# Performance work log

Hardware: AMD Instinct MI355X
Metric: run time of the kernel (lower is better)

Reference implementation:

```python
import jax, jax.numpy as jnp
import numpy as np

EMBED = 1024
HEAD = 128
B, T = 4, 4096


def setup_inputs() -> dict:
    key = jax.random.key(0)
    k1, k2, k3, k4 = jax.random.split(key, 4)
    context = jax.random.normal(k1, (B, T, EMBED), dtype=jnp.float32)
    # nn.Linear(embedding_size, head_size, bias=False): y = x @ W^T; store W^T as [C, H]
    s = 1.0 / np.sqrt(EMBED)
    Wk = jax.random.normal(k2, (EMBED, HEAD), dtype=jnp.float32) * s
    Wq = jax.random.normal(k3, (EMBED, HEAD), dtype=jnp.float32) * s
    Wv = jax.random.normal(k4, (EMBED, HEAD), dtype=jnp.float32) * s
    return {"context": context, "Wk": Wk, "Wq": Wq, "Wv": Wv}


def reference(context, Wk, Wq, Wv):
    Bc, Tc, C = context.shape
    k = jnp.einsum("btc,ch->bth", context, Wk)
    q = jnp.einsum("btc,ch->bth", context, Wq)
    v = jnp.einsum("btc,ch->bth", context, Wv)
    # NOTE: original scales by 1/sqrt(C) (embedding size), not 1/sqrt(head_size)
    scale = 1.0 / jnp.sqrt(jnp.float32(C))
    scores = jnp.einsum("bqh,bkh->bqk", q, k) * scale  # [B, T, T]
    causal = jnp.tril(jnp.ones((Tc, Tc), dtype=bool))
    scores = jnp.where(causal, scores, -jnp.inf)
    attn = jax.nn.softmax(scores, axis=-1)
    # dropout_rate = 0.0 (eval-mode): no-op
    out = jnp.einsum("bqk,bkh->bqh", attn, v)
    return out
```

## Files before the change

kernel.cpp:

```cpp
#include <hip/hip_runtime.h>
#include <cstdint>
#include <cstddef>

#define EMBED 1024
#define HEAD  128
#define BATCH 4
#define SEQ   4096
#define KSC   0.04508422f

typedef __attribute__((ext_vector_type(4))) float f32x4;
typedef __attribute__((ext_vector_type(16))) float f32x16;
typedef __attribute__((ext_vector_type(8))) short s16x8;
typedef __attribute__((ext_vector_type(4))) int i32x4;
typedef __attribute__((ext_vector_type(4))) unsigned short u16x4;

__device__ __forceinline__ unsigned short f2bf(float f) {
    union { float f; unsigned u; } v; v.f = f;
    unsigned r = v.u + 0x7fffu + ((v.u >> 16) & 1u);
    return (unsigned short)(r >> 16);
}

__device__ __forceinline__ int cvtpk(float lo, float hi_) {
    int r;
    asm("v_cvt_pk_bf16_f32 %0, %1, %2" : "=v"(r) : "v"(lo), "v"(hi_));
    return r;
}

__device__ __forceinline__ void gload16(const void* g, void* l) {
    __builtin_amdgcn_global_load_lds(
        (const __attribute__((address_space(1))) unsigned int*)g,
        (__attribute__((address_space(3))) unsigned int*)l, 16, 0, 0);
}

__global__ __launch_bounds__(256) void wt_kernel(const float* __restrict__ Wq,
                                                 const float* __restrict__ Wk,
                                                 const float* __restrict__ Wv,
                                                 unsigned short* __restrict__ Wt) {
    __shared__ __align__(16) float Lw[64 * 132];
    const int tid = threadIdx.x;
    const int sel = blockIdx.x >> 4;
    const int kb  = blockIdx.x & 15;
    const int k0  = kb * 64;
    const float* W = (sel == 0) ? Wq : (sel == 1) ? Wk : Wv;
    #pragma unroll
    for (int it = 0; it < 8; ++it) {
        int c = tid + it * 256;
        int kk = c >> 5, hc = c & 31;
        *(f32x4*)&Lw[kk * 132 + hc * 4] =
            *(const f32x4*)(W + (size_t)(k0 + kk) * HEAD + hc * 4);
    }
    __syncthreads();
    #pragma unroll
    for (int it = 0; it < 4; ++it) {
        int c = tid + it * 256;
        int h = c >> 3, sl = c & 7;
        int phys = sl ^ (h & 7);
        int p0 = cvtpk(Lw[(sl * 8 + 0) * 132 + h], Lw[(sl * 8 + 1) * 132 + h]);
        int p1 = cvtpk(Lw[(sl * 8 + 2) * 132 + h], Lw[(sl * 8 + 3) * 132 + h]);
        int p2 = cvtpk(Lw[(sl * 8 + 4) * 132 + h], Lw[(sl * 8 + 5) * 132 + h]);
        int p3 = cvtpk(Lw[(sl * 8 + 6) * 132 + h], Lw[(sl * 8 + 7) * 132 + h]);
        i32x4 pk = {p0, p1, p2, p3};
        *(s16x8*)(Wt + (size_t)sel * 131072 + kb * 8192 + h * 64 + phys * 8) = *(s16x8*)&pk;
    }
}

__global__ __launch_bounds__(512) void proj_kernel(const float* __restrict__ ctx,
                                                   const unsigned short* __restrict__ Wt,
                                                   unsigned short* __restrict__ Qb,
                                                   unsigned short* __restrict__ Kb,
                                                   unsigned short* __restrict__ Vtb) {
    __shared__ __align__(16) short As[64 * 72];
    __shared__ __align__(16) short Bs[3 * 128 * 64];
    const int tid = threadIdx.x;
    const int lane = tid & 63, w = tid >> 6;
    const int wr = w >> 2, wc = w & 3;
    const int lr = lane & 15, lk = lane >> 4;
    const int m0 = blockIdx.x * 64;

    f32x4 zero = {0.f, 0.f, 0.f, 0.f};
    f32x4 acc[2][6];
    #pragma unroll
    for (int i = 0; i < 2; ++i)
        #pragma unroll
        for (int jn = 0; jn < 6; ++jn) acc[i][jn] = zero;

    for (int kb = 0; kb < 16; ++kb) {
        __syncthreads();
        #pragma unroll
        for (int i = 0; i < 6; ++i) {
            int c = w * 6 + i;
            int sel = c >> 4, within = c & 15;
            gload16((const char*)Wt + sel * 262144 + kb * 16384 + within * 1024 + lane * 16,
                    (char*)Bs + c * 1024);
        }
        {
            int row = tid >> 3, cg = tid & 7;
            const float* src = ctx + (size_t)(m0 + row) * EMBED + kb * 64 + cg * 8;
            f32x4 x0 = *(const f32x4*)src;
            f32x4 x1 = *(const f32x4*)(src + 4);
            int p0 = cvtpk(x0[0], x0[1]);
            int p1 = cvtpk(x0[2], x0[3]);
            int p2 = cvtpk(x1[0], x1[1]);
            int p3 = cvtpk(x1[2], x1[3]);
            i32x4 pk = {p0, p1, p2, p3};
            *(s16x8*)&As[row * 72 + cg * 8] = *(s16x8*)&pk;
        }
        __syncthreads();
        #pragma unroll
        for (int k2 = 0; k2 < 2; ++k2) {
            s16x8 af[2], bfr[6];
            #pragma unroll
            for (int mi = 0; mi < 2; ++mi)
                af[mi] = *(const s16x8*)&As[(wr * 32 + mi * 16 + lr) * 72 + k2 * 32 + lk * 8];
            #pragma unroll
            for (int ni = 0; ni < 6; ++ni) {
                int col = wc * 96 + ni * 16 + lr;
                int sel = col >> 7, rB = col & 127;
                int phys = (k2 * 4 + lk) ^ (rB & 7);
                bfr[ni] = *(const s16x8*)(Bs + sel * 8192 + rB * 64 + phys * 8);
            }
            #pragma unroll
            for (int mi = 0; mi < 2; ++mi)
                #pragma unroll
                for (int ni = 0; ni < 6; ++ni)
                    acc[mi][ni] = __builtin_amdgcn_mfma_f32_16x16x32_bf16(af[mi], bfr[ni], acc[mi][ni], 0, 0, 0);
        }
    }

    #pragma unroll
    for (int mi = 0; mi < 2; ++mi) {
        int rowBase = m0 + wr * 32 + mi * 16 + lk * 4;
        #pragma unroll
        for (int ni = 0; ni < 6; ++ni) {
            int col = wc * 96 + ni * 16 + lr;
            int sel = col >> 7, cIn = col & 127;
            if (sel == 2) {
                int b = rowBase >> 12, tl = rowBase & (SEQ - 1);
                u16x4 vv;
                #pragma unroll
                for (int r = 0; r < 4; ++r) vv[r] = f2bf(acc[mi][ni][r]);
                *(u16x4*)(Vtb + ((size_t)(b * HEAD + cIn)) * SEQ + tl) = vv;
            } else {
                unsigned short* outp = sel ? Kb : Qb;
                float sc = sel ? 1.0f : KSC;
                #pragma unroll
                for (int r = 0; r < 4; ++r)
                    outp[(size_t)(rowBase + r) * HEAD + cIn] = f2bf(acc[mi][ni][r] * sc);
            }
        }
    }
}

__global__ __launch_bounds__(256, 2) void attn_kernel(const unsigned short* __restrict__ Q,
                                                      const unsigned short* __restrict__ K,
                                                      const unsigned short* __restrict__ Vt,
                                                      unsigned short* __restrict__ po,
                                                      float* __restrict__ pml) {
    __shared__ __align__(16) char smem[32768];
    const int tid = threadIdx.x;
    const int lane = tid & 63, w = tid >> 6;
    const int l31 = lane & 31, hi = lane >> 5;
    const int hi16 = hi << 4;

    const int b = blockIdx.x / 272;
    int t = blockIdx.x % 272;
    int qt = 0, cum = 0;
    while (cum + ((qt >> 1) + 1) <= t) { cum += (qt >> 1) + 1; ++qt; }
    const int c = t - cum;
    const int nj = min(4, 2 * qt + 2 - 4 * c);
    const int kb0 = c * 256;
    const int slot = b * 272 + cum + c;

    const unsigned short* qp = Q + ((size_t)(b * SEQ + qt * 128 + w * 32 + l31)) * HEAD + hi * 8;
    s16x8 qf[8];
    #pragma unroll
    for (int dt = 0; dt < 8; ++dt) qf[dt] = *(const s16x8*)(qp + dt * 16);

    f32x16 o0, o1, o2, o3;
    #pragma unroll
    for (int r = 0; r < 16; ++r) { o0[r] = 0.f; o1[r] = 0.f; o2[r] = 0.f; o3[r] = 0.f; }
    float m_run = -1e30f, l_run = 0.f;

    const int krow = tid >> 4, kch = tid & 15;
    const int vdr  = tid >> 3, vch = tid & 7;

    s16x8 kst[4], vst[4];
    #pragma unroll
    for (int p = 0; p < 4; ++p) {
        kst[p] = *(const s16x8*)(K + ((size_t)(b * SEQ + kb0 + krow + p * 16)) * HEAD + kch * 8);
        vst[p] = *(const s16x8*)(Vt + ((size_t)(b * HEAD + vdr + p * 32)) * SEQ + kb0 + vch * 8);
    }
    #pragma unroll
    for (int p = 0; p < 4; ++p) {
        int r0 = krow + p * 16;
        *(s16x8*)(smem + r0 * 256 + ((kch * 16) ^ ((r0 & 7) << 4))) = kst[p];
        int d0 = vdr + p * 32;
        *(s16x8*)(smem + 16384 + d0 * 128 + ((vch * 16) ^ ((d0 & 7) << 4))) = vst[p];
    }
    __syncthreads();

    for (int j = 0; j < nj; ++j) {
        const int kb = kb0 + j * 64;
        if (j + 1 < nj) {
            int kbn = kb + 64;
            #pragma unroll
            for (int p = 0; p < 4; ++p) {
                kst[p] = *(const s16x8*)(K + ((size_t)(b * SEQ + kbn + krow + p * 16)) * HEAD + kch * 8);
                vst[p] = *(const s16x8*)(Vt + ((size_t)(b * HEAD + vdr + p * 32)) * SEQ + kbn + vch * 8);
            }
        }

        f32x16 st0, st1;
        #pragma unroll
        for (int r = 0; r < 16; ++r) { st0[r] = 0.f; st1[r] = 0.f; }
        const int sw = (l31 & 7) << 4;
        const char* kbase0 = smem + l31 * 256;
        const char* kbase1 = kbase0 + 32 * 256;
        __builtin_amdgcn_s_setprio(1);
        #pragma unroll
        for (int dt = 0; dt < 8; ++dt) {
            s16x8 ka0 = *(const s16x8*)(kbase0 + ((dt * 32 + hi16) ^ sw));
            s16x8 ka1 = *(const s16x8*)(kbase1 + ((dt * 32 + hi16) ^ sw));
            st0 = __builtin_amdgcn_mfma_f32_32x32x16_bf16(ka0, qf[dt], st0, 0, 0, 0);
            st1 = __builtin_amdgcn_mfma_f32_32x32x16_bf16(ka1, qf[dt], st1, 0, 0, 0);
        }
        __builtin_amdgcn_s_setprio(0);

        if (4 * c + j >= 2 * qt) {
            const int qg = qt * 128 + w * 32 + l31;
            #pragma unroll
            for (int r = 0; r < 16; ++r) {
                int crow = (r & 3) + 8 * (r >> 2) + 4 * hi;
                if (kb + crow > qg)      st0[r] = -3e37f;
                if (kb + 32 + crow > qg) st1[r] = -3e37f;
            }
        }

        float mx = st0[0];
        #pragma unroll
        for (int r = 1; r < 16; ++r) mx = fmaxf(mx, st0[r]);
        #pragma unroll
        for (int r = 0; r < 16; ++r) mx = fmaxf(mx, st1[r]);
        mx = fmaxf(mx, __shfl_xor(mx, 32));
        if (!__all(mx <= m_run + 8.0f)) {
            float mn = fmaxf(m_run, mx);
            float f = exp2f(m_run - mn);
            l_run *= f;
            int fi = __float_as_int(f);
            #pragma unroll
            for (int r = 0; r < 16; ++r) {
                int srcb = 4 * ((r & 3) + 8 * (r >> 2)) + 16 * hi;
                float fr = __int_as_float(__builtin_amdgcn_ds_bpermute(srcb, fi));
                o0[r] *= fr; o1[r] *= fr; o2[r] *= fr; o3[r] *= fr;
            }
            m_run = mn;
        }
        float rs = 0.f;
        #pragma unroll
        for (int r = 0; r < 16; ++r) {
            st0[r] = exp2f(st0[r] - m_run); rs += st0[r];
            st1[r] = exp2f(st1[r] - m_run); rs += st1[r];
        }
        rs += __shfl_xor(rs, 32);
        l_run += rs;

        int a0 = cvtpk(st0[0], st0[1]),   b0 = cvtpk(st0[4], st0[5]);
        int a1 = cvtpk(st0[2], st0[3]),   b1 = cvtpk(st0[6], st0[7]);
        int a2 = cvtpk(st0[8], st0[9]),   b2 = cvtpk(st0[12], st0[13]);
        int a3 = cvtpk(st0[10], st0[11]), b3 = cvtpk(st0[14], st0[15]);
        int a4 = cvtpk(st1[0], st1[1]),   b4 = cvtpk(st1[4], st1[5]);
        int a5 = cvtpk(st1[2], st1[3]),   b5 = cvtpk(st1[6], st1[7]);
        int a6 = cvtpk(st1[8], st1[9]),   b6 = cvtpk(st1[12], st1[13]);
        int a7 = cvtpk(st1[10], st1[11]), b7 = cvtpk(st1[14], st1[15]);
        asm volatile("v_permlane32_swap_b32 %0, %1" : "+v"(a0), "+v"(b0));
        asm volatile("v_permlane32_swap_b32 %0, %1" : "+v"(a1), "+v"(b1));
        asm volatile("v_permlane32_swap_b32 %0, %1" : "+v"(a2), "+v"(b2));
        asm volatile("v_permlane32_swap_b32 %0, %1" : "+v"(a3), "+v"(b3));
        asm volatile("v_permlane32_swap_b32 %0, %1" : "+v"(a4), "+v"(b4));
        asm volatile("v_permlane32_swap_b32 %0, %1" : "+v"(a5), "+v"(b5));
        asm volatile("v_permlane32_swap_b32 %0, %1" : "+v"(a6), "+v"(b6));
        asm volatile("v_permlane32_swap_b32 %0, %1" : "+v"(a7), "+v"(b7));
        i32x4 pw0 = {a0, a1, b0, b1}; s16x8 pa0 = *(s16x8*)&pw0;
        i32x4 pw1 = {a2, a3, b2, b3}; s16x8 pa1 = *(s16x8*)&pw1;
        i32x4 pw2 = {a4, a5, b4, b5}; s16x8 pa2 = *(s16x8*)&pw2;
        i32x4 pw3 = {a6, a7, b6, b7}; s16x8 pa3 = *(s16x8*)&pw3;

        __builtin_amdgcn_s_setprio(1);
        #define PV_NT(oo, nt) { \
            const int vr = (nt) * 32 + l31; \
            const int vsw = (vr & 7) << 4; \
            const char* vb = smem + 16384 + vr * 128; \
            oo = __builtin_amdgcn_mfma_f32_32x32x16_bf16(pa0, *(const s16x8*)(vb + ((0  + hi16) ^ vsw)), oo, 0, 0, 0); \
            oo = __builtin_amdgcn_mfma_f32_32x32x16_bf16(pa1, *(const s16x8*)(vb + ((32 + hi16) ^ vsw)), oo, 0, 0, 0); \
            oo = __builtin_amdgcn_mfma_f32_32x32x16_bf16(pa2, *(const s16x8*)(vb + ((64 + hi16) ^ vsw)), oo, 0, 0, 0); \
            oo = __builtin_amdgcn_mfma_f32_32x32x16_bf16(pa3, *(const s16x8*)(vb + ((96 + hi16) ^ vsw)), oo, 0, 0, 0); }
        PV_NT(o0, 0) PV_NT(o1, 1) PV_NT(o2, 2) PV_NT(o3, 3)
        #undef PV_NT
        __builtin_amdgcn_s_setprio(0);

        if (j + 1 < nj) {
            __syncthreads();
            #pragma unroll
            for (int p = 0; p < 4; ++p) {
                int r0 = krow + p * 16;
                *(s16x8*)(smem + r0 * 256 + ((kch * 16) ^ ((r0 & 7) << 4))) = kst[p];
                int d0 = vdr + p * 32;
                *(s16x8*)(smem + 16384 + d0 * 128 + ((vch * 16) ^ ((d0 & 7) << 4))) = vst[p];
            }
            __syncthreads();
        }
    }

    __syncthreads();
    short* os = (short*)smem;
    #define STORE_NT(oo, nt) { \
        _Pragma("unroll") \
        for (int r = 0; r < 16; ++r) { \
            int qin = w * 32 + (r & 3) + 8 * (r >> 2) + 4 * hi; \
            os[qin * 128 + (nt) * 32 + l31] = (short)f2bf(oo[r]); \
        } }
    STORE_NT(o0, 0) STORE_NT(o1, 1) STORE_NT(o2, 2) STORE_NT(o3, 3)
    #undef STORE_NT
    unsigned short* pob = po + (size_t)slot * 16384 + w * 4096;
    const short* osw = os + w * 4096;
    #pragma unroll
    for (int jj = 0; jj < 8; ++jj) {
        s16x8 v = *(const s16x8*)(osw + jj * 512 + lane * 8);
        *(s16x8*)(pob + jj * 512 + lane * 8) = v;
    }
    if (lane < 32) {
        float* pm = pml + (size_t)slot * 256 + (w * 32 + lane) * 2;
        pm[0] = m_run; pm[1] = l_run;
    }
}

__global__ __launch_bounds__(256) void combine_kernel(const unsigned short* __restrict__ po,
                                                      const float* __restrict__ pml,
                                                      float* __restrict__ out) {
    const int tid = threadIdx.x;
    const int row = blockIdx.x * 8 + (tid >> 5);
    const int l32 = tid & 31;
    const int b = row >> 12, q = row & 4095;
    const int qt = q >> 7, qr = q & 127;
    const int nc = (q >> 8) + 1;
    const int cum = ((qt >> 1) + (qt & 1)) * ((qt >> 1) + 1);
    const size_t bslot = (size_t)b * 272 + cum;

    float M = -1e30f;
    for (int cc = 0; cc < nc; ++cc)
        M = fmaxf(M, pml[(bslot + cc) * 256 + qr * 2]);
    float L = 0.f;
    f32x4 acc = {0.f, 0.f, 0.f, 0.f};
    for (int cc = 0; cc < nc; ++cc) {
        const float* pm = pml + (bslot + cc) * 256 + qr * 2;
        float wgt = exp2f(pm[0] - M);
        L += wgt * pm[1];
        u16x4 x = *(const u16x4*)(po + (bslot + cc) * 16384 + qr * 128 + l32 * 4);
        #pragma unroll
        for (int e = 0; e < 4; ++e) {
            union { unsigned u; float f; } cv; cv.u = ((unsigned)x[e]) << 16;
            acc[e] += wgt * cv.f;
        }
    }
    float inv = 1.f / L;
    f32x4 y = {acc[0] * inv, acc[1] * inv, acc[2] * inv, acc[3] * inv};
    *(f32x4*)(out + (size_t)row * HEAD + l32 * 4) = y;
}

extern "C" void kernel_launch(void* const* d_in, const int* in_sizes, int n_in,
                              void* d_out, int out_size, void* d_ws, size_t ws_size,
                              hipStream_t stream) {
    const float* ctx = (const float*)d_in[0];
    const float* Wk  = (const float*)d_in[1];
    const float* Wq  = (const float*)d_in[2];
    const float* Wv  = (const float*)d_in[3];
    float* out = (float*)d_out;

    unsigned short* Wt  = (unsigned short*)d_ws;
    unsigned short* Qb  = Wt + 3 * 131072;
    unsigned short* Kb  = Qb + 2097152;
    unsigned short* Vtb = Kb + 2097152;
    unsigned short* po  = Vtb + 2097152;
    float* pml = (float*)(po + (size_t)1088 * 16384);

    wt_kernel<<<48, 256, 0, stream>>>(Wq, Wk, Wv, Wt);
    proj_kernel<<<256, 512, 0, stream>>>(ctx, Wt, Qb, Kb, Vtb);
    attn_kernel<<<1088, 256, 0, stream>>>(Qb, Kb, Vtb, po, pml);
    combine_kernel<<<2048, 256, 0, stream>>>(po, pml, out);
}
```

Before: 171.8 us.

## Fuse split-KV combine into attention via atomic ticket, widen KV chunks

Each attention block now covers up to 512 keys instead of 256, cutting the split count per batch from 272 to 144 work items. The separate combine kernel is removed. The last block to finish a query tile, detected with an atomic counter (reset in wt_kernel), merges the partial outputs and writes the final fp32 result. This removes a kernel launch and some partial-result traffic. The cost is fewer blocks to fill the machine, longer critical-path blocks, and a serial merge tail inside one block per query tile.

```diff
diff --git a/kernel.cpp b/kernel.cpp
--- a/kernel.cpp
+++ b/kernel.cpp
@@ -35,9 +35,11 @@
 __global__ __launch_bounds__(256) void wt_kernel(const float* __restrict__ Wq,
                                                  const float* __restrict__ Wk,
                                                  const float* __restrict__ Wv,
-                                                 unsigned short* __restrict__ Wt) {
+                                                 unsigned short* __restrict__ Wt,
+                                                 int* __restrict__ cnt) {
     __shared__ __align__(16) float Lw[64 * 132];
     const int tid = threadIdx.x;
+    if (blockIdx.x == 0 && tid < 128) cnt[tid] = 0;
     const int sel = blockIdx.x >> 4;
     const int kb  = blockIdx.x & 15;
     const int k0  = kb * 64;
@@ -155,21 +157,25 @@
                                                       const unsigned short* __restrict__ K,
                                                       const unsigned short* __restrict__ Vt,
                                                       unsigned short* __restrict__ po,
-                                                      float* __restrict__ pml) {
+                                                      float* __restrict__ pml,
+                                                      int* __restrict__ cnt,
+                                                      float* __restrict__ out) {
     __shared__ __align__(16) char smem[32768];
+    __shared__ int ticket;
     const int tid = threadIdx.x;
     const int lane = tid & 63, w = tid >> 6;
     const int l31 = lane & 31, hi = lane >> 5;
     const int hi16 = hi << 4;
 
-    const int b = blockIdx.x / 272;
-    int t = blockIdx.x % 272;
-    int qt = 0, cum = 0;
-    while (cum + ((qt >> 1) + 1) <= t) { cum += (qt >> 1) + 1; ++qt; }
+    const int b = blockIdx.x / 144;
+    int t = blockIdx.x % 144;
+    int qt = 0, cum = 0, nc = 1;
+    while (cum + nc <= t) { cum += nc; ++qt; nc = (qt >> 2) + 1; }
     const int c = t - cum;
-    const int nj = min(4, 2 * qt + 2 - 4 * c);
-    const int kb0 = c * 256;
-    const int slot = b * 272 + cum + c;
+    const int nj = min(8, 2 * qt + 2 - 8 * c);
+    const int kb0 = c * 512;
+    const int gbase = b * 144 + cum;
+    const int slot = gbase + c;
 
     const unsigned short* qp = Q + ((size_t)(b * SEQ + qt * 128 + w * 32 + l31)) * HEAD + hi * 8;
     s16x8 qf[8];
@@ -226,7 +232,7 @@
         }
         __builtin_amdgcn_s_setprio(0);
 
-        if (4 * c + j >= 2 * qt) {
+        if (8 * c + j >= 2 * qt) {
             const int qg = qt * 128 + w * 32 + l31;
             #pragma unroll
             for (int r = 0; r < 16; ++r) {
@@ -332,39 +338,36 @@
         float* pm = pml + (size_t)slot * 256 + (w * 32 + lane) * 2;
         pm[0] = m_run; pm[1] = l_run;
     }
-}
-
-__global__ __launch_bounds__(256) void combine_kernel(const unsigned short* __restrict__ po,
-                                                      const float* __restrict__ pml,
-                                                      float* __restrict__ out) {
-    const int tid = threadIdx.x;
-    const int row = blockIdx.x * 8 + (tid >> 5);
-    const int l32 = tid & 31;
-    const int b = row >> 12, q = row & 4095;
-    const int qt = q >> 7, qr = q & 127;
-    const int nc = (q >> 8) + 1;
-    const int cum = ((qt >> 1) + (qt & 1)) * ((qt >> 1) + 1);
-    const size_t bslot = (size_t)b * 272 + cum;
-
-    float M = -1e30f;
-    for (int cc = 0; cc < nc; ++cc)
-        M = fmaxf(M, pml[(bslot + cc) * 256 + qr * 2]);
-    float L = 0.f;
-    f32x4 acc = {0.f, 0.f, 0.f, 0.f};
-    for (int cc = 0; cc < nc; ++cc) {
-        const float* pm = pml + (bslot + cc) * 256 + qr * 2;
-        float wgt = exp2f(pm[0] - M);
-        L += wgt * pm[1];
-        u16x4 x = *(const u16x4*)(po + (bslot + cc) * 16384 + qr * 128 + l32 * 4);
-        #pragma unroll
-        for (int e = 0; e < 4; ++e) {
-            union { unsigned u; float f; } cv; cv.u = ((unsigned)x[e]) << 16;
-            acc[e] += wgt * cv.f;
-        }
-    }
-    float inv = 1.f / L;
-    f32x4 y = {acc[0] * inv, acc[1] * inv, acc[2] * inv, acc[3] * inv};
-    *(f32x4*)(out + (size_t)row * HEAD + l32 * 4) = y;
+
+    __threadfence();
+    if (tid == 0) ticket = atomicAdd(&cnt[b * 32 + qt], 1);
+    __syncthreads();
+    if (ticket == nc - 1) {
+        __threadfence();
+        const int colg = (tid & 31) * 4;
+        for (int it = 0; it < 16; ++it) {
+            int row = it * 8 + (tid >> 5);
+            float M = -1e30f;
+            for (int cc = 0; cc < nc; ++cc)
+                M = fmaxf(M, pml[(size_t)(gbase + cc) * 256 + row * 2]);
+            float L = 0.f;
+            f32x4 acc = {0.f, 0.f, 0.f, 0.f};
+            for (int cc = 0; cc < nc; ++cc) {
+                const float* pm = pml + (size_t)(gbase + cc) * 256 + row * 2;
+                float wgt = exp2f(pm[0] - M);
+                L += wgt * pm[1];
+                u16x4 x = *(const u16x4*)(po + (size_t)(gbase + cc) * 16384 + row * 128 + colg);
+                #pragma unroll
+                for (int e = 0; e < 4; ++e) {
+                    union { unsigned u; float f; } cv; cv.u = ((unsigned)x[e]) << 16;
+                    acc[e] += wgt * cv.f;
+                }
+            }
+            float inv = 1.f / L;
+            f32x4 y = {acc[0] * inv, acc[1] * inv, acc[2] * inv, acc[3] * inv};
+            *(f32x4*)(out + (size_t)(b * SEQ + qt * 128 + row) * HEAD + colg) = y;
+        }
+    }
 }
 
 extern "C" void kernel_launch(void* const* d_in, const int* in_sizes, int n_in,
@@ -381,10 +384,10 @@
     unsigned short* Kb  = Qb + 2097152;
     unsigned short* Vtb = Kb + 2097152;
     unsigned short* po  = Vtb + 2097152;
-    float* pml = (float*)(po + (size_t)1088 * 16384);
-
-    wt_kernel<<<48, 256, 0, stream>>>(Wq, Wk, Wv, Wt);
+    float* pml = (float*)(po + (size_t)576 * 16384);
+    int* cnt   = (int*)(pml + (size_t)576 * 256);
+
+    wt_kernel<<<48, 256, 0, stream>>>(Wq, Wk, Wv, Wt, cnt);
     proj_kernel<<<256, 512, 0, stream>>>(ctx, Wt, Qb, Kb, Vtb);
-    attn_kernel<<<1088, 256, 0, stream>>>(Qb, Kb, Vtb, po, pml);
-    combine_kernel<<<2048, 256, 0, stream>>>(po, pml, out);
-}
+    attn_kernel<<<576, 256, 0, stream>>>(Qb, Kb, Vtb, po, pml, cnt, out);
+}
```

New measurement: 300.5 us. 75.0% more time.
